# Kernel optimization log

Measured on AMD Instinct MI355X. Metric: run time of the kernel, lower is better.

Reference implementation:

```python
import jax, jax.numpy as jnp
import numpy as np

N_NODES = 100_000
N_EDGES = 1_600_000
N_TOKENS = 16
VOCAB = 32_000
TOK_DIM = 64
NODE_DIM = 64
HID = 128
FC = 128
NUM_GRAPHS = 1024


def setup_inputs() -> dict:
    key = jax.random.key(0)
    ks = jax.random.split(key, 14)
    emb = jax.random.normal(ks[0], (VOCAB, TOK_DIM), jnp.float32) * 0.02
    emb = emb.at[0].set(0.0)  # padding_idx=0 row is zero
    return {
        "x_token_idxs": jax.random.randint(ks[1], (N_NODES, N_TOKENS), 0, VOCAB),
        "edge_index": jax.random.randint(ks[2], (2, N_EDGES), 0, N_NODES),
        "batch": jnp.sort(jax.random.randint(ks[3], (N_NODES,), 0, NUM_GRAPHS)),
        "emb": emb,
        "Wp": jax.random.normal(ks[4], (TOK_DIM, NODE_DIM), jnp.float32) * (1.0 / np.sqrt(TOK_DIM)),
        "bp": jnp.zeros((NODE_DIM,), jnp.float32),
        "W1": jax.random.normal(ks[5], (NODE_DIM, HID), jnp.float32) * (1.0 / np.sqrt(NODE_DIM)),
        "b1": jnp.zeros((HID,), jnp.float32),
        "W2": jax.random.normal(ks[6], (HID, HID), jnp.float32) * (1.0 / np.sqrt(HID)),
        "b2": jnp.zeros((HID,), jnp.float32),
        "Wfc": jax.random.normal(ks[7], (HID, FC), jnp.float32) * (1.0 / np.sqrt(HID)),
        "bfc": jnp.zeros((FC,), jnp.float32),
        "Wout": jax.random.normal(ks[8], (FC, 1), jnp.float32) * (1.0 / np.sqrt(FC)),
        "bout": jnp.zeros((1,), jnp.float32),
    }


def reference(x_token_idxs, edge_index, batch, emb, Wp, bp, W1, b1, W2, b2, Wfc, bfc, Wout, bout):
    N = x_token_idxs.shape[0]
    # token embed -> mean pool over tokens -> node projection
    node = emb[x_token_idxs].mean(axis=1) @ Wp + bp  # [N, NODE_DIM]

    # GCN normalization with self-loops (PyG gcn_norm, symmetric)
    loops = jnp.arange(N)
    src = jnp.concatenate([edge_index[0], loops])
    dst = jnp.concatenate([edge_index[1], loops])
    deg = jax.ops.segment_sum(jnp.ones_like(dst, jnp.float32), dst, num_segments=N)
    dis = jnp.where(deg > 0, jax.lax.rsqrt(deg), 0.0)
    norm = (dis[src] * dis[dst])[:, None]  # [E+N, 1]

    def gcn(x, W, b):
        h = x @ W                                      # linear transform first (in->out)
        msg = h[src] * norm                            # gather + scale
        return jax.ops.segment_sum(msg, dst, num_segments=N) + b  # scatter-add + bias

    x = jax.nn.relu(gcn(node, W1, b1))
    x = jax.nn.relu(gcn(x, W2, b2))

    # global mean pool by graph id
    cnt = jax.ops.segment_sum(jnp.ones((N,), jnp.float32), batch, num_segments=NUM_GRAPHS)
    g = jax.ops.segment_sum(x, batch, num_segments=NUM_GRAPHS) / jnp.maximum(cnt, 1.0)[:, None]

    g = jax.nn.relu(g @ Wfc + bfc)
    logits = (g @ Wout + bout).squeeze(-1)  # [NUM_GRAPHS]
    return jax.nn.sigmoid(logits), logits
```

## Files before the change

### kernel.cpp

```cpp
#include <hip/hip_runtime.h>
#include <hip/hip_bf16.h>
#include <hip/hip_fp16.h>
#include <math.h>

#define N_TOKENS 16
#define TOK_DIM 64
#define NODE_DIM 64
#define HID 128
#define FC 128
#define NUM_GRAPHS 1024
#define NBUCK_MAX 512
#define CHUNK 8192

typedef _Float16 f16x8 __attribute__((ext_vector_type(8)));
typedef float f32x4 __attribute__((ext_vector_type(4)));

__device__ __forceinline__ __half2 shfl_xor_h2(__half2 v, int mask) {
    int i = *(int*)&v;
    i = __shfl_xor(i, mask);
    return *(__half2*)&i;
}

__global__ void prep_fused_kernel(const float* __restrict__ Wp, const float* __restrict__ W1,
                                  const float* __restrict__ W2, const float* __restrict__ bp,
                                  const float* __restrict__ emb,
                                  _Float16* __restrict__ Wf16t, _Float16* __restrict__ W2t,
                                  float* __restrict__ bf, __half* __restrict__ emb16, int n4) {
    int b = blockIdx.x;
    int t = threadIdx.x;
    if (b < 128) {
        int n = b;
        if (t < 64) {
            float acc = 0.f;
#pragma unroll
            for (int d = 0; d < 64; d++) acc += Wp[t * 64 + d] * W1[d * 128 + n];
            Wf16t[(size_t)n * 64 + t] = (_Float16)acc;
        } else if (t < 128) {
            int d = t - 64;
            float v = bp[d] * W1[d * 128 + n];
#pragma unroll
            for (int off = 32; off > 0; off >>= 1) v += __shfl_down(v, off);
            if (d == 0) bf[n] = v;
        }
        if (t < 128) W2t[(size_t)n * 128 + t] = (_Float16)W2[(size_t)t * 128 + n];
    } else {
        int i = (b - 128) * 256 + t;
        if (i < n4) {
            float4 v = ((const float4*)emb)[i];
            __half2 h0 = __floats2half2_rn(v.x, v.y);
            __half2 h1 = __floats2half2_rn(v.z, v.w);
            float2 p;
            ((__half2*)&p)[0] = h0;
            ((__half2*)&p)[1] = h1;
            ((float2*)emb16)[i] = p;
        }
    }
}

__global__ void hist_embed_kernel(const int* __restrict__ dst, int* __restrict__ hist2d,
                                  int E, int nbuck, int nchunk,
                                  const int* __restrict__ tok,
                                  const __half* __restrict__ emb16,
                                  __half* __restrict__ mean16, int N) {
    int b = blockIdx.x;
    int t = threadIdx.x;
    if (b < nchunk) {
        __shared__ int h[NBUCK_MAX];
        for (int i = t; i < nbuck; i += 512) h[i] = 0;
        __syncthreads();
        int base = b * CHUNK;
        for (int i = t; i < CHUNK; i += 512) {
            int e = base + i;
            if (e < E) atomicAdd(&h[dst[e] >> 8], 1);
        }
        __syncthreads();
        int* row = hist2d + (size_t)b * NBUCK_MAX;
        for (int i = t; i < nbuck; i += 512) row[i] = h[i];
    } else {
        int w = t >> 6, j = t & 63;
        int q = j >> 3, l = j & 7;
        int i = (b - nchunk) * 8 + w;
        if (i >= N) return;
        const float4* e4 = (const float4*)emb16;
        int t0 = tok[i * 16 + q];
        int t1 = tok[i * 16 + q + 8];
        float4 v0 = e4[(size_t)t0 * 8 + l];
        float4 v1 = e4[(size_t)t1 * 8 + l];
        const __half2* p0 = (const __half2*)&v0;
        const __half2* p1 = (const __half2*)&v1;
        __half2 a0 = __hadd2(p0[0], p1[0]);
        __half2 a1 = __hadd2(p0[1], p1[1]);
        __half2 a2 = __hadd2(p0[2], p1[2]);
        __half2 a3 = __hadd2(p0[3], p1[3]);
#pragma unroll
        for (int mask = 8; mask <= 32; mask <<= 1) {
            a0 = __hadd2(a0, shfl_xor_h2(a0, mask));
            a1 = __hadd2(a1, shfl_xor_h2(a1, mask));
            a2 = __hadd2(a2, shfl_xor_h2(a2, mask));
            a3 = __hadd2(a3, shfl_xor_h2(a3, mask));
        }
        if (q == 0) {
            __half2 inv = __floats2half2_rn(1.0f / 16.0f, 1.0f / 16.0f);
            float4 packed;
            __half2* pp = (__half2*)&packed;
            pp[0] = __hmul2(a0, inv);
            pp[1] = __hmul2(a1, inv);
            pp[2] = __hmul2(a2, inv);
            pp[3] = __hmul2(a3, inv);
            ((float4*)mean16)[(size_t)i * 8 + l] = packed;
        }
    }
}

__global__ void chunk_scan_kernel(const int* __restrict__ hist2d, int* __restrict__ chunkbase,
                                  int* __restrict__ total, int nchunk) {
    int b = blockIdx.x;
    int lane = threadIdx.x;
    int run = 0;
    for (int c0 = 0; c0 < nchunk; c0 += 64) {
        int c = c0 + lane;
        int v = (c < nchunk) ? hist2d[(size_t)c * NBUCK_MAX + b] : 0;
        int s = v;
#pragma unroll
        for (int off = 1; off < 64; off <<= 1) {
            int u = __shfl_up(s, off);
            if (lane >= off) s += u;
        }
        if (c < nchunk) chunkbase[(size_t)c * NBUCK_MAX + b] = s - v + run;
        run += __shfl(s, 63);
    }
    if (lane == 0) total[b] = run;
}

__global__ void binscatter_kernel(const int* __restrict__ src, const int* __restrict__ dst,
                                  const int* __restrict__ total,
                                  const int* __restrict__ chunkbase,
                                  int* __restrict__ bucket_base,
                                  int* __restrict__ staged, int E, int nbuck) {
    __shared__ int s[512];
    __shared__ int h[NBUCK_MAX];
    int t = threadIdx.x;
    int v = (t < nbuck) ? total[t] : 0;
    s[t] = v;
    __syncthreads();
    for (int off = 1; off < 512; off <<= 1) {
        int add = (t >= off) ? s[t - off] : 0;
        __syncthreads();
        s[t] += add;
        __syncthreads();
    }
    const int* cb = chunkbase + (size_t)blockIdx.x * NBUCK_MAX;
    if (t < nbuck) h[t] = (s[t] - v) + cb[t];
    if (blockIdx.x == 0) {
        if (t < nbuck) bucket_base[t] = s[t] - v;
        if (t == 511) bucket_base[nbuck] = s[511];
    }
    __syncthreads();
    int base = blockIdx.x * CHUNK;
    for (int i = t; i < CHUNK; i += 512) {
        int e = base + i;
        if (e < E) {
            int d = dst[e], sv = src[e];
            int b = d >> 8;
            int r = atomicAdd(&h[b], 1);
            staged[r] = sv | ((d & 255) << 17);
        }
    }
}

__global__ void bucket_count_kernel(const int* __restrict__ staged,
                                    const int* __restrict__ bucket_base,
                                    int* __restrict__ row_start, float* __restrict__ dis,
                                    int N, int E) {
    __shared__ int cnt[256];
    __shared__ int sc[256];
    int b = blockIdx.x;
    int t = threadIdx.x;
    cnt[t] = 0;
    __syncthreads();
    int rb0 = bucket_base[b], rb1 = bucket_base[b + 1];
    for (int i = rb0 + t; i < rb1; i += 256) atomicAdd(&cnt[staged[i] >> 17], 1);
    __syncthreads();
    int v = cnt[t];
    sc[t] = v;
    __syncthreads();
    for (int off = 1; off < 256; off <<= 1) {
        int add = (t >= off) ? sc[t - off] : 0;
        __syncthreads();
        sc[t] += add;
        __syncthreads();
    }
    int node = b * 256 + t;
    if (node < N) {
        row_start[node] = rb0 + sc[t] - v;
        dis[node] = rsqrtf(1.0f + (float)v);
    }
    if (b == 0 && t == 0) row_start[N] = E;
}

__global__ void csr_write_kernel(const int* __restrict__ staged,
                                 const int* __restrict__ bucket_base,
                                 const int* __restrict__ row_start,
                                 const float* __restrict__ dis,
                                 int2* __restrict__ csr, float* __restrict__ rowsum, int N) {
    __shared__ int cur[256];
    __shared__ float dl[256];
    __shared__ float wsum[256];
    int b = blockIdx.x;
    int t = threadIdx.x;
    int node = b * 256 + t;
    cur[t] = (node < N) ? row_start[node] : 0;
    dl[t] = (node < N) ? dis[node] : 0.f;
    wsum[t] = 0.f;
    __syncthreads();
    int rb0 = bucket_base[b], rb1 = bucket_base[b + 1];
    for (int i = rb0 + t; i < rb1; i += 256) {
        int v = staged[i];
        int s = v & 131071;
        int dloc = v >> 17;
        float w = dis[s] * dl[dloc];
        int pos = atomicAdd(&cur[dloc], 1);
        __half2 wh = __floats2half2_rn(w, w);
        csr[pos] = make_int2(s, *(int*)&wh);
        atomicAdd(&wsum[dloc], w);
    }
    __syncthreads();
    if (node < N) rowsum[node] = wsum[t] + dl[t] * dl[t];
}

#define NB 32
__global__ __launch_bounds__(256, 6)
void agg64_dense_kernel(const __half* __restrict__ mean16,
                        const int* __restrict__ row_start,
                        const int2* __restrict__ csr,
                        const float* __restrict__ dis,
                        const float* __restrict__ rowsum,
                        const _Float16* __restrict__ Wf16t,
                        const float* __restrict__ bf,
                        const float* __restrict__ b1,
                        const _Float16* __restrict__ W2t,
                        __half* __restrict__ h2, int N) {
    __shared__ _Float16 sagg[32][72];
    __shared__ _Float16 sx1[32][136];
    __shared__ float srs[32];
    int t = threadIdx.x;
    int nb0 = blockIdx.x * NB;
    const float4* m4 = (const float4*)mean16;

    if (t < 32) srs[t] = (nb0 + t < N) ? rowsum[nb0 + t] : 0.f;

    {
        int nl = t >> 3;
        int l = t & 7;
        int node = nb0 + nl;
        __half2 a0, a1, a2, a3;
        a0 = a1 = a2 = a3 = __floats2half2_rn(0.f, 0.f);
        if (node < N) {
            int beg = row_start[node];
            int end = row_start[node + 1];
            float d = dis[node];
            {
                float4 raw = m4[(size_t)node * 8 + l];
                const __half2* hp = (const __half2*)&raw;
                float d2f = d * d;
                __half2 d2h = __floats2half2_rn(d2f, d2f);
                a0 = __hmul2(hp[0], d2h); a1 = __hmul2(hp[1], d2h);
                a2 = __hmul2(hp[2], d2h); a3 = __hmul2(hp[3], d2h);
            }
            int k = beg;
            int kfull = beg + ((end - beg) & ~7);
            for (; k < kfull; k += 8) {
                int2 e[8];
                float4 v[8];
#pragma unroll
                for (int m = 0; m < 8; m++) e[m] = csr[k + m];
#pragma unroll
                for (int m = 0; m < 8; m++) v[m] = m4[(size_t)e[m].x * 8 + l];
#pragma unroll
                for (int m = 0; m < 8; m++) {
                    __half2 wh = *(__half2*)&e[m].y;
                    const __half2* hp = (const __half2*)&v[m];
                    a0 = __hfma2(hp[0], wh, a0);
                    a1 = __hfma2(hp[1], wh, a1);
                    a2 = __hfma2(hp[2], wh, a2);
                    a3 = __hfma2(hp[3], wh, a3);
                }
            }
            if (k < end) {
                int2 e[8];
                float4 v[8];
#pragma unroll
                for (int m = 0; m < 8; m++) {
                    int kk = k + m;
                    e[m] = (kk < end) ? csr[kk] : make_int2(0, 0);
                }
#pragma unroll
                for (int m = 0; m < 8; m++) v[m] = m4[(size_t)e[m].x * 8 + l];
#pragma unroll
                for (int m = 0; m < 8; m++) {
                    __half2 wh = *(__half2*)&e[m].y;
                    const __half2* hp = (const __half2*)&v[m];
                    a0 = __hfma2(hp[0], wh, a0);
                    a1 = __hfma2(hp[1], wh, a1);
                    a2 = __hfma2(hp[2], wh, a2);
                    a3 = __hfma2(hp[3], wh, a3);
                }
            }
        }
        float4 packed;
        __half2* pp = (__half2*)&packed;
        pp[0] = a0; pp[1] = a1; pp[2] = a2; pp[3] = a3;
        *(float4*)(&sagg[nl][l * 8]) = packed;
    }
    __syncthreads();

    int wv = t >> 6, lane = t & 63;
    int rh = wv & 1;
    int ncb = (wv >> 1) * 64;
    int m16 = lane & 15;
    int qq = lane >> 4;

    f32x4 c0 = {}, c1 = {}, c2 = {}, c3 = {};
#pragma unroll
    for (int ks = 0; ks < 2; ks++) {
        int k0 = ks * 32 + qq * 8;
        f16x8 afrag = *(const f16x8*)(&sagg[rh * 16 + m16][k0]);
        f16x8 b0 = *(const f16x8*)(Wf16t + (size_t)(ncb + 0 * 16 + m16) * 64 + k0);
        f16x8 b1f = *(const f16x8*)(Wf16t + (size_t)(ncb + 1 * 16 + m16) * 64 + k0);
        f16x8 b2f = *(const f16x8*)(Wf16t + (size_t)(ncb + 2 * 16 + m16) * 64 + k0);
        f16x8 b3f = *(const f16x8*)(Wf16t + (size_t)(ncb + 3 * 16 + m16) * 64 + k0);
        c0 = __builtin_amdgcn_mfma_f32_16x16x32_f16(afrag, b0, c0, 0, 0, 0);
        c1 = __builtin_amdgcn_mfma_f32_16x16x32_f16(afrag, b1f, c1, 0, 0, 0);
        c2 = __builtin_amdgcn_mfma_f32_16x16x32_f16(afrag, b2f, c2, 0, 0, 0);
        c3 = __builtin_amdgcn_mfma_f32_16x16x32_f16(afrag, b3f, c3, 0, 0, 0);
    }
    {
        f32x4 cc[4] = {c0, c1, c2, c3};
#pragma unroll
        for (int nt = 0; nt < 4; nt++) {
            int ncol = ncb + nt * 16 + m16;
            float bfj = bf[ncol], b1j = b1[ncol];
#pragma unroll
            for (int r = 0; r < 4; r++) {
                int mrow = qq * 4 + r;
                float z = cc[nt][r] + srs[rh * 16 + mrow] * bfj + b1j;
                sx1[rh * 16 + mrow][ncol] = (_Float16)fmaxf(z, 0.f);
            }
        }
    }
    __syncthreads();

    f32x4 d0 = {}, d1 = {}, d2 = {}, d3 = {};
#pragma unroll
    for (int ks = 0; ks < 4; ks++) {
        int k0 = ks * 32 + qq * 8;
        f16x8 afrag = *(const f16x8*)(&sx1[rh * 16 + m16][k0]);
        f16x8 b0 = *(const f16x8*)(W2t + (size_t)(ncb + 0 * 16 + m16) * 128 + k0);
        f16x8 b1f = *(const f16x8*)(W2t + (size_t)(ncb + 1 * 16 + m16) * 128 + k0);
        f16x8 b2f = *(const f16x8*)(W2t + (size_t)(ncb + 2 * 16 + m16) * 128 + k0);
        f16x8 b3f = *(const f16x8*)(W2t + (size_t)(ncb + 3 * 16 + m16) * 128 + k0);
        d0 = __builtin_amdgcn_mfma_f32_16x16x32_f16(afrag, b0, d0, 0, 0, 0);
        d1 = __builtin_amdgcn_mfma_f32_16x16x32_f16(afrag, b1f, d1, 0, 0, 0);
        d2 = __builtin_amdgcn_mfma_f32_16x16x32_f16(afrag, b2f, d2, 0, 0, 0);
        d3 = __builtin_amdgcn_mfma_f32_16x16x32_f16(afrag, b3f, d3, 0, 0, 0);
    }
    {
        f32x4 dd[4] = {d0, d1, d2, d3};
#pragma unroll
        for (int nt = 0; nt < 4; nt++) {
            int ncol = ncb + nt * 16 + m16;
#pragma unroll
            for (int r = 0; r < 4; r++) {
                int node = nb0 + rh * 16 + qq * 4 + r;
                if (node < N) h2[(size_t)node * 128 + ncol] = __float2half(dd[nt][r]);
            }
        }
    }
}

__global__ __launch_bounds__(256, 8)
void gcn_agg128_kernel(const __half* __restrict__ hsrc,
                       const int* __restrict__ row_start,
                       const int2* __restrict__ csr,
                       const float* __restrict__ dis,
                       const float* __restrict__ b2,
                       __half* __restrict__ outx, int N) {
    int t = threadIdx.x;
    int w = t >> 6, j = t & 63;
    int q = j >> 4, l = j & 15;
    int node = blockIdx.x * 4 + w;
    if (node >= N) return;
    const float4* h4 = (const float4*)hsrc;
    int beg = row_start[node];
    int end = row_start[node + 1];
    float d = dis[node];
    __half2 a0, a1, a2, a3;
    {
        float4 raw = h4[(size_t)node * 16 + l];
        const __half2* hp = (const __half2*)&raw;
        float d2f = d * d * ((q == 0) ? 1.f : 0.f);
        __half2 d2h = __floats2half2_rn(d2f, d2f);
        a0 = __hmul2(hp[0], d2h); a1 = __hmul2(hp[1], d2h);
        a2 = __hmul2(hp[2], d2h); a3 = __hmul2(hp[3], d2h);
    }
    int k = beg;
    int kfull = beg + ((end - beg) & ~31);
    for (; k < kfull; k += 32) {
        int2 e[8];
        float4 v[8];
#pragma unroll
        for (int m = 0; m < 8; m++) e[m] = csr[k + 4 * m + q];
#pragma unroll
        for (int m = 0; m < 8; m++) v[m] = h4[(size_t)e[m].x * 16 + l];
#pragma unroll
        for (int m = 0; m < 8; m++) {
            __half2 wh = *(__half2*)&e[m].y;
            const __half2* hp = (const __half2*)&v[m];
            a0 = __hfma2(hp[0], wh, a0);
            a1 = __hfma2(hp[1], wh, a1);
            a2 = __hfma2(hp[2], wh, a2);
            a3 = __hfma2(hp[3], wh, a3);
        }
    }
    if (k < end) {
        int2 e[8];
        float4 v[8];
#pragma unroll
        for (int m = 0; m < 8; m++) {
            int kk = k + 4 * m + q;
            e[m] = (kk < end) ? csr[kk] : make_int2(0, 0);
        }
#pragma unroll
        for (int m = 0; m < 8; m++) v[m] = h4[(size_t)e[m].x * 16 + l];
#pragma unroll
        for (int m = 0; m < 8; m++) {
            __half2 wh = *(__half2*)&e[m].y;
            const __half2* hp = (const __half2*)&v[m];
            a0 = __hfma2(hp[0], wh, a0);
            a1 = __hfma2(hp[1], wh, a1);
            a2 = __hfma2(hp[2], wh, a2);
            a3 = __hfma2(hp[3], wh, a3);
        }
    }
#pragma unroll
    for (int mask = 16; mask <= 32; mask <<= 1) {
        a0 = __hadd2(a0, shfl_xor_h2(a0, mask));
        a1 = __hadd2(a1, shfl_xor_h2(a1, mask));
        a2 = __hadd2(a2, shfl_xor_h2(a2, mask));
        a3 = __hadd2(a3, shfl_xor_h2(a3, mask));
    }
    if (q == 0) {
        float2 f0 = __half22float2(a0), f1 = __half22float2(a1);
        float2 f2 = __half22float2(a2), f3 = __half22float2(a3);
        const float4* b4 = (const float4*)b2;
        float4 ba = b4[l * 2], bb = b4[l * 2 + 1];
        __half2 o0 = __floats2half2_rn(fmaxf(f0.x + ba.x, 0.f), fmaxf(f0.y + ba.y, 0.f));
        __half2 o1 = __floats2half2_rn(fmaxf(f1.x + ba.z, 0.f), fmaxf(f1.y + ba.w, 0.f));
        __half2 o2 = __floats2half2_rn(fmaxf(f2.x + bb.x, 0.f), fmaxf(f2.y + bb.y, 0.f));
        __half2 o3 = __floats2half2_rn(fmaxf(f3.x + bb.z, 0.f), fmaxf(f3.y + bb.w, 0.f));
        float4 packed;
        __half2* pp = (__half2*)&packed;
        pp[0] = o0; pp[1] = o1; pp[2] = o2; pp[3] = o3;
        ((float4*)outx)[(size_t)node * 16 + l] = packed;
    }
}

__device__ __forceinline__ int lower_bound_i(const int* __restrict__ a, int n, int val) {
    int lo = 0, hi = n;
    while (lo < hi) {
        int mid = (lo + hi) >> 1;
        if (a[mid] < val) lo = mid + 1; else hi = mid;
    }
    return lo;
}

__global__ void pool_head_kernel(const __half* __restrict__ x,
                                 const int* __restrict__ batch,
                                 const float* __restrict__ Wfc,
                                 const float* __restrict__ bfc,
                                 const float* __restrict__ Wout,
                                 const float* __restrict__ bout,
                                 float* __restrict__ out, int N) {
    int gr = blockIdx.x;
    int t = threadIdx.x;
    int j2 = t & 63, w = t >> 6;
    __shared__ float2 spart[4][64];
    __shared__ float sg[128];
    __shared__ float sfc[2][128];
    __shared__ float sred[128];
    int beg = lower_bound_i(batch, N, gr);
    int end = lower_bound_i(batch, N, gr + 1);
    const __half2* x2 = (const __half2*)x;
    float2 acc = make_float2(0.f, 0.f);
    for (int i = beg + w; i < end; i += 4) {
        float2 a = __half22float2(x2[(size_t)i * 64 + j2]);
        acc.x += a.x; acc.y += a.y;
    }
    spart[w][j2] = acc;
    __syncthreads();
    if (t < 64) {
        float inv = 1.0f / fmaxf((float)(end - beg), 1.0f);
        float2 s0 = spart[0][t], s1 = spart[1][t];
        float2 s2 = spart[2][t], s3 = spart[3][t];
        sg[2 * t] = (s0.x + s1.x + s2.x + s3.x) * inv;
        sg[2 * t + 1] = (s0.y + s1.y + s2.y + s3.y) * inv;
    }
    __syncthreads();
    int j = t & 127, hb = t >> 7;
    float a = 0.f;
#pragma unroll
    for (int k = 0; k < 64; k++) a += sg[hb * 64 + k] * Wfc[(hb * 64 + k) * 128 + j];
    sfc[hb][j] = a;
    __syncthreads();
    if (t < 128) {
        float aa = sfc[0][t] + sfc[1][t] + bfc[t];
        float f = fmaxf(aa, 0.f);
        sred[t] = f * Wout[t];
    }
    __syncthreads();
    if (t < 64) {
        float v = sred[t] + sred[t + 64];
#pragma unroll
        for (int off = 32; off > 0; off >>= 1) v += __shfl_down(v, off);
        if (t == 0) {
            float logit = v + bout[0];
            out[gr] = 1.0f / (1.0f + expf(-logit));
            out[NUM_GRAPHS + gr] = logit;
        }
    }
}

extern "C" void kernel_launch(void* const* d_in, const int* in_sizes, int n_in,
                              void* d_out, int out_size, void* d_ws, size_t ws_size,
                              hipStream_t stream) {
    const int* tok   = (const int*)d_in[0];
    const int* eidx  = (const int*)d_in[1];
    const int* batch = (const int*)d_in[2];
    const float* emb = (const float*)d_in[3];
    const float* Wp  = (const float*)d_in[4];
    const float* bp  = (const float*)d_in[5];
    const float* W1  = (const float*)d_in[6];
    const float* b1  = (const float*)d_in[7];
    const float* W2  = (const float*)d_in[8];
    const float* b2  = (const float*)d_in[9];
    const float* Wfc = (const float*)d_in[10];
    const float* bfc = (const float*)d_in[11];
    const float* Wout= (const float*)d_in[12];
    const float* bout= (const float*)d_in[13];
    float* out = (float*)d_out;

    const int N = in_sizes[2];
    const int E = in_sizes[1] / 2;
    const int* src = eidx;
    const int* dst = eidx + E;
    const int Np = (N + 3) & ~3;
    const int nbuck = (N + 255) / 256;
    const int nchunk = (E + CHUNK - 1) / CHUNK;
    const int emb_n4 = in_sizes[3] / 4;

    float* ws = (float*)d_ws;
    size_t off = 0;
    float* dis     = ws + off;            off += Np;
    __half* mean16 = (__half*)(ws + off); off += (size_t)Np * 32;
    __half* agg16  = (__half*)(ws + off); off += (size_t)Np * 32;
    float* rowsum  = ws + off;            off += Np;
    __half* h2buf  = (__half*)(ws + off); off += (size_t)Np * 64;
    __half* xfin16 = (__half*)(ws + off); off += (size_t)Np * 64;
    __half* emb16  = (__half*)(ws + off); off += (size_t)(in_sizes[3] / 2 + 4);
    _Float16* Wf16t = (_Float16*)(ws + off); off += 4096;
    _Float16* W2t   = (_Float16*)(ws + off); off += 8192;
    float* bf      = ws + off;            off += 128;
    int* row_start = (int*)(ws + off);    off += Np + 4;
    int* staged    = (int*)(ws + off);    off += E;
    int* total     = (int*)(ws + off);    off += NBUCK_MAX;
    int* bucket_base   = (int*)(ws + off); off += NBUCK_MAX + 8;
    int2* csr      = (int2*)(ws + off);
    int* hist2d    = (int*)h2buf;
    int* chunkbase = hist2d + (size_t)nchunk * NBUCK_MAX;

    prep_fused_kernel<<<128 + (emb_n4 + 255) / 256, 256, 0, stream>>>(
        Wp, W1, W2, bp, emb, Wf16t, W2t, bf, emb16, emb_n4);

    hist_embed_kernel<<<nchunk + (N + 7) / 8, 512, 0, stream>>>(
        dst, hist2d, E, nbuck, nchunk, tok, emb16, mean16, N);

    chunk_scan_kernel<<<nbuck, 64, 0, stream>>>(hist2d, chunkbase, total, nchunk);

    binscatter_kernel<<<nchunk, 512, 0, stream>>>(src, dst, total, chunkbase,
                                                  bucket_base, staged, E, nbuck);

    bucket_count_kernel<<<nbuck, 256, 0, stream>>>(staged, bucket_base, row_start, dis, N, E);
    csr_write_kernel<<<nbuck, 256, 0, stream>>>(staged, bucket_base, row_start, dis,
                                                csr, rowsum, N);

    agg64_dense_kernel<<<(N + NB - 1) / NB, 256, 0, stream>>>(mean16, row_start, csr, dis,
                                                              rowsum, Wf16t, bf, b1, W2t,
                                                              h2buf, N);

    gcn_agg128_kernel<<<(N + 3) / 4, 256, 0, stream>>>(h2buf, row_start, csr, dis, b2,
                                                       xfin16, N);

    pool_head_kernel<<<NUM_GRAPHS, 256, 0, stream>>>(xfin16, batch, Wfc, bfc, Wout, bout,
                                                     out, N);
}
```

Baseline: 302.9 us.

## Compute node degrees via global atomics and merge bucket count into CSR write

Per-node in-degrees are now counted with global atomics in the histogram pass, after being zeroed in the prep kernel. dis is computed in the chunk scan, and the separate bucket-count kernel is folded into a merged CSR-write kernel that recomputes bucket bases from totals. This removes one kernel launch and one full pass over the staged edges. In exchange it adds 1.6M global atomics on the deg array and a redundant 512-wide scan in every CSR block.

```diff
diff --git a/kernel.cpp b/kernel.cpp
--- a/kernel.cpp
+++ b/kernel.cpp
@@ -25,7 +25,8 @@
                                   const float* __restrict__ W2, const float* __restrict__ bp,
                                   const float* __restrict__ emb,
                                   _Float16* __restrict__ Wf16t, _Float16* __restrict__ W2t,
-                                  float* __restrict__ bf, __half* __restrict__ emb16, int n4) {
+                                  float* __restrict__ bf, __half* __restrict__ emb16, int n4,
+                                  int embB, int* __restrict__ deg, int ndeg) {
     int b = blockIdx.x;
     int t = threadIdx.x;
     if (b < 128) {
@@ -43,7 +44,7 @@
             if (d == 0) bf[n] = v;
         }
         if (t < 128) W2t[(size_t)n * 128 + t] = (_Float16)W2[(size_t)t * 128 + n];
-    } else {
+    } else if (b < 128 + embB) {
         int i = (b - 128) * 256 + t;
         if (i < n4) {
             float4 v = ((const float4*)emb)[i];
@@ -54,11 +55,14 @@
             ((__half2*)&p)[1] = h1;
             ((float2*)emb16)[i] = p;
         }
+    } else {
+        int i = (b - 128 - embB) * 256 + t;
+        if (i < ndeg) deg[i] = 0;
     }
 }
 
 __global__ void hist_embed_kernel(const int* __restrict__ dst, int* __restrict__ hist2d,
-                                  int E, int nbuck, int nchunk,
+                                  int E, int nbuck, int nchunk, int* __restrict__ deg,
                                   const int* __restrict__ tok,
                                   const __half* __restrict__ emb16,
                                   __half* __restrict__ mean16, int N) {
@@ -71,7 +75,11 @@
         int base = b * CHUNK;
         for (int i = t; i < CHUNK; i += 512) {
             int e = base + i;
-            if (e < E) atomicAdd(&h[dst[e] >> 8], 1);
+            if (e < E) {
+                int d = dst[e];
+                atomicAdd(&h[d >> 8], 1);
+                atomicAdd(&deg[d], 1);
+            }
         }
         __syncthreads();
         int* row = hist2d + (size_t)b * NBUCK_MAX;
@@ -113,7 +121,8 @@
 }
 
 __global__ void chunk_scan_kernel(const int* __restrict__ hist2d, int* __restrict__ chunkbase,
-                                  int* __restrict__ total, int nchunk) {
+                                  int* __restrict__ total, int nchunk,
+                                  const int* __restrict__ deg, float* __restrict__ dis, int N) {
     int b = blockIdx.x;
     int lane = threadIdx.x;
     int run = 0;
@@ -130,12 +139,17 @@
         run += __shfl(s, 63);
     }
     if (lane == 0) total[b] = run;
+    int nb = b * 256;
+#pragma unroll
+    for (int i = 0; i < 4; i++) {
+        int node = nb + lane + i * 64;
+        if (node < N) dis[node] = rsqrtf(1.0f + (float)deg[node]);
+    }
 }
 
 __global__ void binscatter_kernel(const int* __restrict__ src, const int* __restrict__ dst,
                                   const int* __restrict__ total,
                                   const int* __restrict__ chunkbase,
-                                  int* __restrict__ bucket_base,
                                   int* __restrict__ staged, int E, int nbuck) {
     __shared__ int s[512];
     __shared__ int h[NBUCK_MAX];
@@ -151,10 +165,6 @@
     }
     const int* cb = chunkbase + (size_t)blockIdx.x * NBUCK_MAX;
     if (t < nbuck) h[t] = (s[t] - v) + cb[t];
-    if (blockIdx.x == 0) {
-        if (t < nbuck) bucket_base[t] = s[t] - v;
-        if (t == 511) bucket_base[nbuck] = s[511];
-    }
     __syncthreads();
     int base = blockIdx.x * CHUNK;
     for (int i = t; i < CHUNK; i += 512) {
@@ -168,64 +178,66 @@
     }
 }
 
-__global__ void bucket_count_kernel(const int* __restrict__ staged,
-                                    const int* __restrict__ bucket_base,
-                                    int* __restrict__ row_start, float* __restrict__ dis,
-                                    int N, int E) {
-    __shared__ int cnt[256];
+__global__ void csr_merged_kernel(const int* __restrict__ staged,
+                                  const int* __restrict__ total,
+                                  const int* __restrict__ deg,
+                                  const float* __restrict__ dis,
+                                  int* __restrict__ row_start,
+                                  int2* __restrict__ csr, float* __restrict__ rowsum,
+                                  int N, int E, int nbuck) {
+    __shared__ int s[512];
     __shared__ int sc[256];
-    int b = blockIdx.x;
-    int t = threadIdx.x;
-    cnt[t] = 0;
-    __syncthreads();
-    int rb0 = bucket_base[b], rb1 = bucket_base[b + 1];
-    for (int i = rb0 + t; i < rb1; i += 256) atomicAdd(&cnt[staged[i] >> 17], 1);
-    __syncthreads();
-    int v = cnt[t];
-    sc[t] = v;
-    __syncthreads();
-    for (int off = 1; off < 256; off <<= 1) {
-        int add = (t >= off) ? sc[t - off] : 0;
-        __syncthreads();
-        sc[t] += add;
-        __syncthreads();
-    }
-    int node = b * 256 + t;
-    if (node < N) {
-        row_start[node] = rb0 + sc[t] - v;
-        dis[node] = rsqrtf(1.0f + (float)v);
-    }
-    if (b == 0 && t == 0) row_start[N] = E;
-}
-
-__global__ void csr_write_kernel(const int* __restrict__ staged,
-                                 const int* __restrict__ bucket_base,
-                                 const int* __restrict__ row_start,
-                                 const float* __restrict__ dis,
-                                 int2* __restrict__ csr, float* __restrict__ rowsum, int N) {
     __shared__ int cur[256];
     __shared__ float dl[256];
     __shared__ float wsum[256];
     int b = blockIdx.x;
     int t = threadIdx.x;
+    int v = (t < nbuck) ? total[t] : 0;
+    s[t] = v;
+    __syncthreads();
+    for (int off = 1; off < 512; off <<= 1) {
+        int add = (t >= off) ? s[t - off] : 0;
+        __syncthreads();
+        s[t] += add;
+        __syncthreads();
+    }
+    int myTot = total[b];
+    int rb0 = s[b] - myTot;
+    int rb1 = rb0 + myTot;
     int node = b * 256 + t;
-    cur[t] = (node < N) ? row_start[node] : 0;
-    dl[t] = (node < N) ? dis[node] : 0.f;
-    wsum[t] = 0.f;
-    __syncthreads();
-    int rb0 = bucket_base[b], rb1 = bucket_base[b + 1];
-    for (int i = rb0 + t; i < rb1; i += 256) {
-        int v = staged[i];
-        int s = v & 131071;
-        int dloc = v >> 17;
-        float w = dis[s] * dl[dloc];
+    int dv = 0;
+    if (t < 256) {
+        dv = (node < N) ? deg[node] : 0;
+        sc[t] = dv;
+    }
+    __syncthreads();
+    for (int off = 1; off < 256; off <<= 1) {
+        int add = (t < 256 && t >= off) ? sc[t - off] : 0;
+        __syncthreads();
+        if (t < 256) sc[t] += add;
+        __syncthreads();
+    }
+    if (t < 256) {
+        int rs = rb0 + sc[t] - dv;
+        if (node < N) row_start[node] = rs;
+        cur[t] = rs;
+        dl[t] = (node < N) ? dis[node] : 0.f;
+        wsum[t] = 0.f;
+    }
+    if (b == 0 && t == 0) row_start[N] = E;
+    __syncthreads();
+    for (int i = rb0 + t; i < rb1; i += 512) {
+        int v2 = staged[i];
+        int sidx = v2 & 131071;
+        int dloc = v2 >> 17;
+        float w = dis[sidx] * dl[dloc];
         int pos = atomicAdd(&cur[dloc], 1);
         __half2 wh = __floats2half2_rn(w, w);
-        csr[pos] = make_int2(s, *(int*)&wh);
+        csr[pos] = make_int2(sidx, *(int*)&wh);
         atomicAdd(&wsum[dloc], w);
     }
     __syncthreads();
-    if (node < N) rowsum[node] = wsum[t] + dl[t] * dl[t];
+    if (t < 256 && node < N) rowsum[node] = wsum[t] + dl[t] * dl[t];
 }
 
 #define NB 32
@@ -557,6 +569,8 @@
     const int nbuck = (N + 255) / 256;
     const int nchunk = (E + CHUNK - 1) / CHUNK;
     const int emb_n4 = in_sizes[3] / 4;
+    const int embB = (emb_n4 + 255) / 256;
+    const int degB = (Np + 255) / 256;
 
     float* ws = (float*)d_ws;
     size_t off = 0;
@@ -575,23 +589,25 @@
     int* total     = (int*)(ws + off);    off += NBUCK_MAX;
     int* bucket_base   = (int*)(ws + off); off += NBUCK_MAX + 8;
     int2* csr      = (int2*)(ws + off);
+    (void)bucket_base;
+    int* deg = (int*)agg16;
     int* hist2d    = (int*)h2buf;
     int* chunkbase = hist2d + (size_t)nchunk * NBUCK_MAX;
 
-    prep_fused_kernel<<<128 + (emb_n4 + 255) / 256, 256, 0, stream>>>(
-        Wp, W1, W2, bp, emb, Wf16t, W2t, bf, emb16, emb_n4);
+    prep_fused_kernel<<<128 + embB + degB, 256, 0, stream>>>(
+        Wp, W1, W2, bp, emb, Wf16t, W2t, bf, emb16, emb_n4, embB, deg, Np);
 
     hist_embed_kernel<<<nchunk + (N + 7) / 8, 512, 0, stream>>>(
-        dst, hist2d, E, nbuck, nchunk, tok, emb16, mean16, N);
-
-    chunk_scan_kernel<<<nbuck, 64, 0, stream>>>(hist2d, chunkbase, total, nchunk);
+        dst, hist2d, E, nbuck, nchunk, deg, tok, emb16, mean16, N);
+
+    chunk_scan_kernel<<<nbuck, 64, 0, stream>>>(hist2d, chunkbase, total, nchunk,
+                                                deg, dis, N);
 
     binscatter_kernel<<<nchunk, 512, 0, stream>>>(src, dst, total, chunkbase,
-                                                  bucket_base, staged, E, nbuck);
-
-    bucket_count_kernel<<<nbuck, 256, 0, stream>>>(staged, bucket_base, row_start, dis, N, E);
-    csr_write_kernel<<<nbuck, 256, 0, stream>>>(staged, bucket_base, row_start, dis,
-                                                csr, rowsum, N);
+                                                  staged, E, nbuck);
+
+    csr_merged_kernel<<<nbuck, 512, 0, stream>>>(staged, total, deg, dis, row_start,
+                                                 csr, rowsum, N, E, nbuck);
 
     agg64_dense_kernel<<<(N + NB - 1) / NB, 256, 0, stream>>>(mean16, row_start, csr, dis,
                                                               rowsum, Wf16t, bf, b1, W2t,
```

Result: slower. 359.8 us (+18.8%).

## Pack CSR entries into 32-bit words with source index and half dis weight

Applied to the files above, without the earlier changes.

Each CSR entry shrinks from an int2 (source index plus a half2 weight) to one 32-bit word holding the 17-bit source index and the upper 15 bits of the half-precision dis[src]. The destination normalization dis[dst] is moved out of the per-edge weight and applied once per node after aggregation, in both aggregation kernels. This halves CSR read and write traffic in the bandwidth-bound gather loops. It costs a few extra bit ops per edge and relies on dis being positive and node ids fitting in 17 bits.

```diff
diff --git a/kernel.cpp b/kernel.cpp
--- a/kernel.cpp
+++ b/kernel.cpp
@@ -19,6 +19,12 @@
     int i = *(int*)&v;
     i = __shfl_xor(i, mask);
     return *(__half2*)&i;
+}
+
+__device__ __forceinline__ void unpack_csr(unsigned e, unsigned& s, __half2& wh) {
+    s = e & 131071u;
+    __half hd = __ushort_as_half((unsigned short)(e >> 17));
+    wh = __halves2half2(hd, hd);
 }
 
 __global__ void prep_fused_kernel(const float* __restrict__ Wp, const float* __restrict__ W1,
@@ -202,7 +208,7 @@
                                  const int* __restrict__ bucket_base,
                                  const int* __restrict__ row_start,
                                  const float* __restrict__ dis,
-                                 int2* __restrict__ csr, float* __restrict__ rowsum, int N) {
+                                 int* __restrict__ csr, float* __restrict__ rowsum, int N) {
     __shared__ int cur[256];
     __shared__ float dl[256];
     __shared__ float wsum[256];
@@ -218,10 +224,10 @@
         int v = staged[i];
         int s = v & 131071;
         int dloc = v >> 17;
-        float w = dis[s] * dl[dloc];
+        __half hds = __float2half_rn(dis[s]);
+        float w = __half2float(hds) * dl[dloc];
         int pos = atomicAdd(&cur[dloc], 1);
-        __half2 wh = __floats2half2_rn(w, w);
-        csr[pos] = make_int2(s, *(int*)&wh);
+        csr[pos] = s | ((int)(__half_as_ushort(hds) & 0x7FFF) << 17);
         atomicAdd(&wsum[dloc], w);
     }
     __syncthreads();
@@ -232,7 +238,7 @@
 __global__ __launch_bounds__(256, 6)
 void agg64_dense_kernel(const __half* __restrict__ mean16,
                         const int* __restrict__ row_start,
-                        const int2* __restrict__ csr,
+                        const int* __restrict__ csr,
                         const float* __restrict__ dis,
                         const float* __restrict__ rowsum,
                         const _Float16* __restrict__ Wf16t,
@@ -246,6 +252,7 @@
     int t = threadIdx.x;
     int nb0 = blockIdx.x * NB;
     const float4* m4 = (const float4*)mean16;
+    const unsigned* csru = (const unsigned*)csr;
 
     if (t < 32) srs[t] = (nb0 + t < N) ? rowsum[nb0 + t] : 0.f;
 
@@ -255,30 +262,31 @@
         int node = nb0 + nl;
         __half2 a0, a1, a2, a3;
         a0 = a1 = a2 = a3 = __floats2half2_rn(0.f, 0.f);
+        float d = 0.f;
         if (node < N) {
             int beg = row_start[node];
             int end = row_start[node + 1];
-            float d = dis[node];
+            d = dis[node];
             {
                 float4 raw = m4[(size_t)node * 8 + l];
                 const __half2* hp = (const __half2*)&raw;
-                float d2f = d * d;
-                __half2 d2h = __floats2half2_rn(d2f, d2f);
-                a0 = __hmul2(hp[0], d2h); a1 = __hmul2(hp[1], d2h);
-                a2 = __hmul2(hp[2], d2h); a3 = __hmul2(hp[3], d2h);
+                __half2 dh = __floats2half2_rn(d, d);
+                a0 = __hmul2(hp[0], dh); a1 = __hmul2(hp[1], dh);
+                a2 = __hmul2(hp[2], dh); a3 = __hmul2(hp[3], dh);
             }
             int k = beg;
             int kfull = beg + ((end - beg) & ~7);
             for (; k < kfull; k += 8) {
-                int2 e[8];
+                unsigned e[8];
                 float4 v[8];
 #pragma unroll
-                for (int m = 0; m < 8; m++) e[m] = csr[k + m];
-#pragma unroll
-                for (int m = 0; m < 8; m++) v[m] = m4[(size_t)e[m].x * 8 + l];
+                for (int m = 0; m < 8; m++) e[m] = csru[k + m];
+#pragma unroll
+                for (int m = 0; m < 8; m++) v[m] = m4[(size_t)(e[m] & 131071u) * 8 + l];
 #pragma unroll
                 for (int m = 0; m < 8; m++) {
-                    __half2 wh = *(__half2*)&e[m].y;
+                    unsigned s; __half2 wh;
+                    unpack_csr(e[m], s, wh);
                     const __half2* hp = (const __half2*)&v[m];
                     a0 = __hfma2(hp[0], wh, a0);
                     a1 = __hfma2(hp[1], wh, a1);
@@ -287,18 +295,19 @@
                 }
             }
             if (k < end) {
-                int2 e[8];
+                unsigned e[8];
                 float4 v[8];
 #pragma unroll
                 for (int m = 0; m < 8; m++) {
                     int kk = k + m;
-                    e[m] = (kk < end) ? csr[kk] : make_int2(0, 0);
+                    e[m] = (kk < end) ? csru[kk] : 0u;
                 }
 #pragma unroll
-                for (int m = 0; m < 8; m++) v[m] = m4[(size_t)e[m].x * 8 + l];
+                for (int m = 0; m < 8; m++) v[m] = m4[(size_t)(e[m] & 131071u) * 8 + l];
 #pragma unroll
                 for (int m = 0; m < 8; m++) {
-                    __half2 wh = *(__half2*)&e[m].y;
+                    unsigned s; __half2 wh;
+                    unpack_csr(e[m], s, wh);
                     const __half2* hp = (const __half2*)&v[m];
                     a0 = __hfma2(hp[0], wh, a0);
                     a1 = __hfma2(hp[1], wh, a1);
@@ -307,6 +316,9 @@
                 }
             }
         }
+        __half2 dh2 = __floats2half2_rn(d, d);
+        a0 = __hmul2(a0, dh2); a1 = __hmul2(a1, dh2);
+        a2 = __hmul2(a2, dh2); a3 = __hmul2(a3, dh2);
         float4 packed;
         __half2* pp = (__half2*)&packed;
         pp[0] = a0; pp[1] = a1; pp[2] = a2; pp[3] = a3;
@@ -381,7 +393,7 @@
 __global__ __launch_bounds__(256, 8)
 void gcn_agg128_kernel(const __half* __restrict__ hsrc,
                        const int* __restrict__ row_start,
-                       const int2* __restrict__ csr,
+                       const int* __restrict__ csr,
                        const float* __restrict__ dis,
                        const float* __restrict__ b2,
                        __half* __restrict__ outx, int N) {
@@ -391,6 +403,7 @@
     int node = blockIdx.x * 4 + w;
     if (node >= N) return;
     const float4* h4 = (const float4*)hsrc;
+    const unsigned* csru = (const unsigned*)csr;
     int beg = row_start[node];
     int end = row_start[node + 1];
     float d = dis[node];
@@ -398,23 +411,24 @@
     {
         float4 raw = h4[(size_t)node * 16 + l];
         const __half2* hp = (const __half2*)&raw;
-        float d2f = d * d * ((q == 0) ? 1.f : 0.f);
-        __half2 d2h = __floats2half2_rn(d2f, d2f);
-        a0 = __hmul2(hp[0], d2h); a1 = __hmul2(hp[1], d2h);
-        a2 = __hmul2(hp[2], d2h); a3 = __hmul2(hp[3], d2h);
+        float df = d * ((q == 0) ? 1.f : 0.f);
+        __half2 dh = __floats2half2_rn(df, df);
+        a0 = __hmul2(hp[0], dh); a1 = __hmul2(hp[1], dh);
+        a2 = __hmul2(hp[2], dh); a3 = __hmul2(hp[3], dh);
     }
     int k = beg;
     int kfull = beg + ((end - beg) & ~31);
     for (; k < kfull; k += 32) {
-        int2 e[8];
+        unsigned e[8];
         float4 v[8];
 #pragma unroll
-        for (int m = 0; m < 8; m++) e[m] = csr[k + 4 * m + q];
-#pragma unroll
-        for (int m = 0; m < 8; m++) v[m] = h4[(size_t)e[m].x * 16 + l];
+        for (int m = 0; m < 8; m++) e[m] = csru[k + 4 * m + q];
+#pragma unroll
+        for (int m = 0; m < 8; m++) v[m] = h4[(size_t)(e[m] & 131071u) * 16 + l];
 #pragma unroll
         for (int m = 0; m < 8; m++) {
-            __half2 wh = *(__half2*)&e[m].y;
+            unsigned s; __half2 wh;
+            unpack_csr(e[m], s, wh);
             const __half2* hp = (const __half2*)&v[m];
             a0 = __hfma2(hp[0], wh, a0);
             a1 = __hfma2(hp[1], wh, a1);
@@ -423,18 +437,19 @@
         }
     }
     if (k < end) {
-        int2 e[8];
+        unsigned e[8];
         float4 v[8];
 #pragma unroll
         for (int m = 0; m < 8; m++) {
             int kk = k + 4 * m + q;
-            e[m] = (kk < end) ? csr[kk] : make_int2(0, 0);
-        }
-#pragma unroll
-        for (int m = 0; m < 8; m++) v[m] = h4[(size_t)e[m].x * 16 + l];
+            e[m] = (kk < end) ? csru[kk] : 0u;
+        }
+#pragma unroll
+        for (int m = 0; m < 8; m++) v[m] = h4[(size_t)(e[m] & 131071u) * 16 + l];
 #pragma unroll
         for (int m = 0; m < 8; m++) {
-            __half2 wh = *(__half2*)&e[m].y;
+            unsigned s; __half2 wh;
+            unpack_csr(e[m], s, wh);
             const __half2* hp = (const __half2*)&v[m];
             a0 = __hfma2(hp[0], wh, a0);
             a1 = __hfma2(hp[1], wh, a1);
@@ -454,10 +469,10 @@
         float2 f2 = __half22float2(a2), f3 = __half22float2(a3);
         const float4* b4 = (const float4*)b2;
         float4 ba = b4[l * 2], bb = b4[l * 2 + 1];
-        __half2 o0 = __floats2half2_rn(fmaxf(f0.x + ba.x, 0.f), fmaxf(f0.y + ba.y, 0.f));
-        __half2 o1 = __floats2half2_rn(fmaxf(f1.x + ba.z, 0.f), fmaxf(f1.y + ba.w, 0.f));
-        __half2 o2 = __floats2half2_rn(fmaxf(f2.x + bb.x, 0.f), fmaxf(f2.y + bb.y, 0.f));
-        __half2 o3 = __floats2half2_rn(fmaxf(f3.x + bb.z, 0.f), fmaxf(f3.y + bb.w, 0.f));
+        __half2 o0 = __floats2half2_rn(fmaxf(f0.x * d + ba.x, 0.f), fmaxf(f0.y * d + ba.y, 0.f));
+        __half2 o1 = __floats2half2_rn(fmaxf(f1.x * d + ba.z, 0.f), fmaxf(f1.y * d + ba.w, 0.f));
+        __half2 o2 = __floats2half2_rn(fmaxf(f2.x * d + bb.x, 0.f), fmaxf(f2.y * d + bb.y, 0.f));
+        __half2 o3 = __floats2half2_rn(fmaxf(f3.x * d + bb.z, 0.f), fmaxf(f3.y * d + bb.w, 0.f));
         float4 packed;
         __half2* pp = (__half2*)&packed;
         pp[0] = o0; pp[1] = o1; pp[2] = o2; pp[3] = o3;
@@ -574,7 +589,7 @@
     int* staged    = (int*)(ws + off);    off += E;
     int* total     = (int*)(ws + off);    off += NBUCK_MAX;
     int* bucket_base   = (int*)(ws + off); off += NBUCK_MAX + 8;
-    int2* csr      = (int2*)(ws + off);
+    int* csr       = (int*)(ws + off);
     int* hist2d    = (int*)h2buf;
     int* chunkbase = hist2d + (size_t)nchunk * NBUCK_MAX;
 
```

Measured after the change: 294.4 us. -2.8%, faster.
